# Optimization experiments

Measured on AMD Instinct MI355X. Metric: run time of the kernel, lower is better.

## Reference

```python
import jax, jax.numpy as jnp
import numpy as np

WIDTH = 256
BASE = 4
BUTTERFLY_COUNT = 4  # 256 == 4**4


def butterfly_permutation(width, group_size, multiplier):
    """Fixed channel permutation from ButterflyPermutation (kernel_size=1)."""
    batch_size = group_size * multiplier
    idx = np.arange(width)
    idx_in_group = idx % group_size
    group_idx = (idx % batch_size) // group_size
    batch_idx = (idx % width) // batch_size
    return group_idx + multiplier * idx_in_group + batch_size * batch_idx


# permutation after butterfly conv i (i = 0,1,2): group_size = base**(i+1), multiplier = base
PERMS = [butterfly_permutation(WIDTH, BASE ** (i + 1), BASE) for i in range(BUTTERFLY_COUNT - 1)]


def gconv1x1(x, w):
    """Grouped 1x1 conv. x: [B, G*I, H, W]; w: [G, O, I] -> [B, G*O, H, W]."""
    B, C, H, Wd = x.shape
    G, O, I = w.shape
    xg = x.reshape(B, G, I, H, Wd)
    y = jnp.einsum('goi,bgihw->bgohw', w, xg)
    return y.reshape(B, G * O, H, Wd)


def setup_inputs() -> dict:
    key = jax.random.key(0)
    ks = jax.random.split(key, 5)
    B, C, H, W = 32, WIDTH, 56, 56
    G, O, I = 64, 4, 4
    scale = 1.0 / np.sqrt(I)
    x = jax.random.normal(ks[0], (B, C, H, W), dtype=jnp.float32)
    ws = [jax.random.normal(ks[i + 1], (G, O, I), dtype=jnp.float32) * scale for i in range(4)]
    return {"x": x, "w0": ws[0], "w1": ws[1], "w2": ws[2], "w3": ws[3]}


def reference(x, w0, w1, w2, w3):
    # butterfly chain: conv -> perm -> conv -> perm -> conv -> perm -> conv
    weights = [w0, w1, w2, w3]
    for i in range(BUTTERFLY_COUNT):
        x = gconv1x1(x, weights[i])
        if i != BUTTERFLY_COUNT - 1:
            x = x[:, PERMS[i], :, :]
    return x
```

## Files before the change

kernel.cpp:

```cpp
#include <hip/hip_runtime.h>


#define NPIX_TILE 64
#define NTILES_PER_IMG 49
#define HW 3136

__global__ __launch_bounds__(1024, 4)
void butterfly_fused_kernel(const float* __restrict__ x,
                            const float* __restrict__ w0,
                            const float* __restrict__ w1,
                            const float* __restrict__ w2,
                            const float* __restrict__ w3,
                            float* __restrict__ out) {
    __shared__ float buf[256][NPIX_TILE];

    const int p   = threadIdx.x & 63;
    const int set = __builtin_amdgcn_readfirstlane((int)(threadIdx.x >> 6));
    const int img  = blockIdx.x / NTILES_PER_IMG;
    const int tile = blockIdx.x % NTILES_PER_IMG;
    const int base = img * 256 * HW + tile * NPIX_TILE + p;

    const int u = set >> 2, v = set & 3;

    float xr[16];
#pragma unroll
    for (int i = 0; i < 4; ++i)
#pragma unroll
        for (int j = 0; j < 4; ++j) {
            const int c = (u << 6) | (v << 4) | (i << 2) | j;
            xr[4 * i + j] = x[base + c * HW];
        }

    float b0[16];
#pragma unroll
    for (int i = 0; i < 4; ++i) {
        const float* wg = w0 + (((u << 4) | (v << 2) | i) << 4);
#pragma unroll
        for (int o = 0; o < 4; ++o) {
            float acc = wg[o * 4 + 0] * xr[4 * i + 0];
            acc += wg[o * 4 + 1] * xr[4 * i + 1];
            acc += wg[o * 4 + 2] * xr[4 * i + 2];
            acc += wg[o * 4 + 3] * xr[4 * i + 3];
            b0[4 * i + o] = acc;
        }
    }

    float b1[16];
#pragma unroll
    for (int d1 = 0; d1 < 4; ++d1) {
        const float* wg = w1 + (((u << 4) | (v << 2) | d1) << 4);
#pragma unroll
        for (int o = 0; o < 4; ++o) {
            float acc = wg[o * 4 + 0] * b0[0 + d1];
            acc += wg[o * 4 + 1] * b0[4 + d1];
            acc += wg[o * 4 + 2] * b0[8 + d1];
            acc += wg[o * 4 + 3] * b0[12 + d1];
            b1[4 * d1 + o] = acc;
        }
    }

#pragma unroll
    for (int k = 0; k < 16; ++k)
        buf[(set << 4) | k][p] = b1[k];

    __syncthreads();

    const int e = u, f = v;

    float yr[16];
#pragma unroll
    for (int i = 0; i < 4; ++i)
#pragma unroll
        for (int i2 = 0; i2 < 4; ++i2)
            yr[4 * i + i2] = buf[(e << 6) | (i << 4) | (i2 << 2) | f][p];

    float b2[16];
#pragma unroll
    for (int i = 0; i < 4; ++i) {
        const float* wg = w2 + (((e << 4) | (f << 2) | i) << 4);
#pragma unroll
        for (int o = 0; o < 4; ++o) {
            float acc = wg[o * 4 + 0] * yr[4 * i + 0];
            acc += wg[o * 4 + 1] * yr[4 * i + 1];
            acc += wg[o * 4 + 2] * yr[4 * i + 2];
            acc += wg[o * 4 + 3] * yr[4 * i + 3];
            b2[4 * i + o] = acc;
        }
    }

#pragma unroll
    for (int g2 = 0; g2 < 4; ++g2) {
        const float* wg = w3 + (((g2 << 4) | (e << 2) | f) << 4);
#pragma unroll
        for (int o = 0; o < 4; ++o) {
            float acc = wg[o * 4 + 0] * b2[0 + g2];
            acc += wg[o * 4 + 1] * b2[4 + g2];
            acc += wg[o * 4 + 2] * b2[8 + g2];
            acc += wg[o * 4 + 3] * b2[12 + g2];
            const int c = (g2 << 6) | (e << 4) | (f << 2) | o;
            out[base + c * HW] = acc;
        }
    }
}

extern "C" void kernel_launch(void* const* d_in, const int* in_sizes, int n_in,
                              void* d_out, int out_size, void* d_ws, size_t ws_size,
                              hipStream_t stream) {
    const float* x  = (const float*)d_in[0];
    const float* w0 = (const float*)d_in[1];
    const float* w1 = (const float*)d_in[2];
    const float* w2 = (const float*)d_in[3];
    const float* w3 = (const float*)d_in[4];
    float* out = (float*)d_out;

    dim3 grid(32 * NTILES_PER_IMG);
    dim3 block(1024);
    butterfly_fused_kernel<<<grid, block, 0, stream>>>(x, w0, w1, w2, w3, out);
}
```

Measured before the change: 38.80 us.

## Vectorize pixels as float4 and split blocks by channel quarter

Each thread now processes four contiguous pixels using float4 global loads, shared-memory accesses and nontemporal float4 stores. The grid is also split by the top channel quarter, which the permutation structure shows is independent, so blocks shrink to 256 threads with a 64-channel shared buffer. The aim is fewer memory instructions and lighter block-wide synchronisation. It adds a partial final tile that needs a bounds guard, and raises register pressure from the 4-wide arrays.

```diff
diff --git a/kernel.cpp b/kernel.cpp
--- a/kernel.cpp
+++ b/kernel.cpp
@@ -1,89 +1,98 @@
 #include <hip/hip_runtime.h>
 
 
-#define NPIX_TILE 64
-#define NTILES_PER_IMG 49
 #define HW 3136
+#define TILE_PX 256
+#define NT 13
 
-__global__ __launch_bounds__(1024, 4)
-void butterfly_fused_kernel(const float* __restrict__ x,
-                            const float* __restrict__ w0,
-                            const float* __restrict__ w1,
-                            const float* __restrict__ w2,
-                            const float* __restrict__ w3,
-                            float* __restrict__ out) {
-    __shared__ float buf[256][NPIX_TILE];
+typedef float f32x4 __attribute__((ext_vector_type(4)));
 
-    const int p   = threadIdx.x & 63;
-    const int set = __builtin_amdgcn_readfirstlane((int)(threadIdx.x >> 6));
-    const int img  = blockIdx.x / NTILES_PER_IMG;
-    const int tile = blockIdx.x % NTILES_PER_IMG;
-    const int base = img * 256 * HW + tile * NPIX_TILE + p;
+__device__ __forceinline__ void fma4(f32x4& acc, float s, const f32x4& a) {
+    acc = s * a + acc;
+}
 
-    const int u = set >> 2, v = set & 3;
+__global__ __launch_bounds__(256, 2)
+void butterfly_fused_v2(const float* __restrict__ x,
+                        const float* __restrict__ w0,
+                        const float* __restrict__ w1,
+                        const float* __restrict__ w2,
+                        const float* __restrict__ w3,
+                        float* __restrict__ out) {
+    __shared__ float buf[64 * TILE_PX];
 
-    float xr[16];
+    const int l  = threadIdx.x & 63;
+    const int wv = __builtin_amdgcn_readfirstlane((int)(threadIdx.x >> 6));
+    const int bid  = blockIdx.x;
+    const int tile = bid % NT;
+    const int rem  = bid / NT;
+    const int e    = rem & 3;
+    const int img  = rem >> 2;
+
+    const int pix  = tile * TILE_PX + 4 * l;
+    const bool ok  = pix < HW;
+    const int pixc = ok ? pix : 0;
+    const int ibase = img * 256 * HW + pixc;
+    const int obase = img * 256 * HW + pix;
+
+    f32x4 xr[16];
 #pragma unroll
     for (int i = 0; i < 4; ++i)
 #pragma unroll
         for (int j = 0; j < 4; ++j) {
-            const int c = (u << 6) | (v << 4) | (i << 2) | j;
-            xr[4 * i + j] = x[base + c * HW];
+            const int c = (e << 6) | (wv << 4) | (i << 2) | j;
+            xr[4 * i + j] = *reinterpret_cast<const f32x4*>(x + ibase + c * HW);
         }
 
-    float b0[16];
+    f32x4 b0[16];
 #pragma unroll
     for (int i = 0; i < 4; ++i) {
-        const float* wg = w0 + (((u << 4) | (v << 2) | i) << 4);
+        const float* wg = w0 + (((e << 4) | (wv << 2) | i) << 4);
 #pragma unroll
         for (int o = 0; o < 4; ++o) {
-            float acc = wg[o * 4 + 0] * xr[4 * i + 0];
-            acc += wg[o * 4 + 1] * xr[4 * i + 1];
-            acc += wg[o * 4 + 2] * xr[4 * i + 2];
-            acc += wg[o * 4 + 3] * xr[4 * i + 3];
+            f32x4 acc = wg[o * 4 + 0] * xr[4 * i + 0];
+            fma4(acc, wg[o * 4 + 1], xr[4 * i + 1]);
+            fma4(acc, wg[o * 4 + 2], xr[4 * i + 2]);
+            fma4(acc, wg[o * 4 + 3], xr[4 * i + 3]);
             b0[4 * i + o] = acc;
         }
     }
 
-    float b1[16];
 #pragma unroll
     for (int d1 = 0; d1 < 4; ++d1) {
-        const float* wg = w1 + (((u << 4) | (v << 2) | d1) << 4);
+        const float* wg = w1 + (((e << 4) | (wv << 2) | d1) << 4);
 #pragma unroll
         for (int o = 0; o < 4; ++o) {
-            float acc = wg[o * 4 + 0] * b0[0 + d1];
-            acc += wg[o * 4 + 1] * b0[4 + d1];
-            acc += wg[o * 4 + 2] * b0[8 + d1];
-            acc += wg[o * 4 + 3] * b0[12 + d1];
-            b1[4 * d1 + o] = acc;
+            f32x4 acc = wg[o * 4 + 0] * b0[0 + d1];
+            fma4(acc, wg[o * 4 + 1], b0[4 + d1]);
+            fma4(acc, wg[o * 4 + 2], b0[8 + d1]);
+            fma4(acc, wg[o * 4 + 3], b0[12 + d1]);
+            const int lc = (wv << 4) | (d1 << 2) | o;
+            *reinterpret_cast<f32x4*>(buf + lc * TILE_PX + 4 * l) = acc;
         }
     }
 
-#pragma unroll
-    for (int k = 0; k < 16; ++k)
-        buf[(set << 4) | k][p] = b1[k];
-
     __syncthreads();
 
-    const int e = u, f = v;
-
-    float yr[16];
+    const int f = wv;
+    f32x4 yr[16];
 #pragma unroll
     for (int i = 0; i < 4; ++i)
 #pragma unroll
-        for (int i2 = 0; i2 < 4; ++i2)
-            yr[4 * i + i2] = buf[(e << 6) | (i << 4) | (i2 << 2) | f][p];
+        for (int i2 = 0; i2 < 4; ++i2) {
+            const int lc = (i << 4) | (i2 << 2) | f;
+            yr[4 * i + i2] = *reinterpret_cast<const f32x4*>(buf + lc * TILE_PX + 4 * l);
+        }
 
-    float b2[16];
+    f32x4 b2[16];
 #pragma unroll
     for (int i = 0; i < 4; ++i) {
         const float* wg = w2 + (((e << 4) | (f << 2) | i) << 4);
 #pragma unroll
         for (int o = 0; o < 4; ++o) {
-            float acc = wg[o * 4 + 0] * yr[4 * i + 0];
-            acc += wg[o * 4 + 1] * yr[4 * i + 1];
-            acc += wg[o * 4 + 2] * yr[4 * i + 2];
-            acc += wg[o * 4 + 3] * yr[4 * i + 3];
+            f32x4 acc = wg[o * 4 + 0] * yr[4 * i + 0];
+            fma4(acc, wg[o * 4 + 1], yr[4 * i + 1]);
+            fma4(acc, wg[o * 4 + 2], yr[4 * i + 2]);
+            fma4(acc, wg[o * 4 + 3], yr[4 * i + 3]);
             b2[4 * i + o] = acc;
         }
     }
@@ -93,12 +102,15 @@
         const float* wg = w3 + (((g2 << 4) | (e << 2) | f) << 4);
 #pragma unroll
         for (int o = 0; o < 4; ++o) {
-            float acc = wg[o * 4 + 0] * b2[0 + g2];
-            acc += wg[o * 4 + 1] * b2[4 + g2];
-            acc += wg[o * 4 + 2] * b2[8 + g2];
-            acc += wg[o * 4 + 3] * b2[12 + g2];
-            const int c = (g2 << 6) | (e << 4) | (f << 2) | o;
-            out[base + c * HW] = acc;
+            f32x4 acc = wg[o * 4 + 0] * b2[0 + g2];
+            fma4(acc, wg[o * 4 + 1], b2[4 + g2]);
+            fma4(acc, wg[o * 4 + 2], b2[8 + g2]);
+            fma4(acc, wg[o * 4 + 3], b2[12 + g2]);
+            if (ok) {
+                const int c = (g2 << 6) | (e << 4) | (f << 2) | o;
+                __builtin_nontemporal_store(acc,
+                    reinterpret_cast<f32x4*>(out + obase + c * HW));
+            }
         }
     }
 }
@@ -113,7 +125,7 @@
     const float* w3 = (const float*)d_in[4];
     float* out = (float*)d_out;
 
-    dim3 grid(32 * NTILES_PER_IMG);
-    dim3 block(1024);
-    butterfly_fused_kernel<<<grid, block, 0, stream>>>(x, w0, w1, w2, w3, out);
+    dim3 grid(32 * 4 * NT);
+    dim3 block(256);
+    butterfly_fused_v2<<<grid, block, 0, stream>>>(x, w0, w1, w2, w3, out);
 }
```

After: 38.80 us. No clear change (-0.0%).
